# Performance work log

Measured on AMD Instinct MI355X. Metric: run time of the kernel, lower is better.

## Reference

```python
import jax, jax.numpy as jnp
import numpy as np
from jax import lax

B, C, O, K, KS, H, W = 16, 256, 256, 4, 3, 64, 64
PAD = 1
BN_EPS = 1e-3


def setup_inputs() -> dict:
    key = jax.random.key(0)
    k1, k2, k3 = jax.random.split(key, 3)
    x = jax.random.normal(k1, (B, C, H, W), dtype=jnp.float32)
    # nn.Parameter(torch.randn(...)) -> standard normal init
    dyn_kernels = jax.random.normal(k2, (K, O, C, KS, KS), dtype=jnp.float32)
    # attention 1x1 conv (no bias): weight [K, C, 1, 1] -> store as [K, C]
    attn_w = jax.random.normal(k3, (K, C), dtype=jnp.float32) / np.sqrt(C).astype(np.float32)
    gamma = jnp.ones((O,), dtype=jnp.float32)
    beta = jnp.zeros((O,), dtype=jnp.float32)
    return {"x": x, "dyn_kernels": dyn_kernels, "attn_w": attn_w, "gamma": gamma, "beta": beta}


def reference(x, dyn_kernels, attn_w, gamma, beta):
    b, c, h, w = x.shape
    k, o = dyn_kernels.shape[0], dyn_kernels.shape[1]
    # attention: global avg pool -> 1x1 conv (no bias) -> softmax over kernels
    pooled = x.mean(axis=(2, 3))                      # [B, C]
    attn = jax.nn.softmax(pooled @ attn_w.T, axis=1)  # [B, K]
    # run all K kernels as a single conv with K*O output channels
    kern = dyn_kernels.reshape(k * o, c, KS, KS)
    y = lax.conv_general_dilated(
        x, kern, window_strides=(1, 1), padding=((PAD, PAD), (PAD, PAD)),
        dimension_numbers=("NCHW", "OIHW", "NCHW"))   # [B, K*O, H, W]
    y = y.reshape(b, k, o, h, w)
    out = jnp.einsum("bkohw,bk->bohw", y, attn)        # weighted sum over kernels
    # BatchNorm2d (training mode: batch statistics, biased variance)
    mean = out.mean(axis=(0, 2, 3))
    var = out.var(axis=(0, 2, 3))
    inv = gamma * lax.rsqrt(var + BN_EPS)
    out = (out - mean[None, :, None, None]) * inv[None, :, None, None] + beta[None, :, None, None]
    # SiLU
    return out * jax.nn.sigmoid(out)
```

## Files before the change

### kernel.cpp

```cpp
#include <hip/hip_runtime.h>
#include <math.h>


#define B_ 16
#define C_ 256
#define O_ 256
#define HW_ 4096
#define PLANE_F4 1024
#define WPERK 589824
#define XS_PX 40

typedef short bf16x8 __attribute__((ext_vector_type(8)));
typedef float f32x4 __attribute__((ext_vector_type(4)));

__device__ __forceinline__ unsigned short f2bf(float f) {
    unsigned u = __float_as_uint(f);
    u += 0x7FFFu + ((u >> 16) & 1u);
    return (unsigned short)(u >> 16);
}
__device__ __forceinline__ float bf2f(unsigned short h) {
    return __uint_as_float((unsigned)h << 16);
}

__global__ __launch_bounds__(256) void pool_kernel(const float4* __restrict__ x4,
                                                   float* __restrict__ pooled) {
    int bc = blockIdx.x;
    const float4* p = x4 + (size_t)bc * PLANE_F4;
    float s = 0.f;
    for (int i = threadIdx.x; i < PLANE_F4; i += 256) {
        float4 v = p[i];
        s += v.x + v.y + v.z + v.w;
    }
    for (int off = 32; off; off >>= 1) s += __shfl_down(s, off);
    __shared__ float partial[4];
    if ((threadIdx.x & 63) == 0) partial[threadIdx.x >> 6] = s;
    __syncthreads();
    if (threadIdx.x == 0)
        pooled[bc] = (partial[0] + partial[1] + partial[2] + partial[3]) * (1.f / 4096.f);
}

__global__ void attn_kernel(const float* __restrict__ pooled,
                            const float* __restrict__ attn_w,
                            float* __restrict__ attn) {
    int tid = threadIdx.x;
    int b = tid >> 2, k = tid & 3;
    float s = 0.f;
    for (int c = 0; c < C_; ++c) s += pooled[b * C_ + c] * attn_w[k * C_ + c];
    __shared__ float lg[16][4];
    lg[b][k] = s;
    __syncthreads();
    float m = fmaxf(fmaxf(lg[b][0], lg[b][1]), fmaxf(lg[b][2], lg[b][3]));
    float den = expf(lg[b][0] - m) + expf(lg[b][1] - m) +
                expf(lg[b][2] - m) + expf(lg[b][3] - m);
    attn[tid] = expf(s - m) / den;
}

__global__ __launch_bounds__(256) void wtrans_kernel(const float* __restrict__ dyn,
                                                     const float* __restrict__ attn,
                                                     unsigned short* __restrict__ wt_hi,
                                                     unsigned short* __restrict__ wt_lo) {
    int idx = blockIdx.x * 256 + threadIdx.x;
    int b = idx >> 16;
    int o = (idx >> 8) & 255;
    int c = idx & 255;
    float a0 = attn[b * 4 + 0], a1 = attn[b * 4 + 1],
          a2 = attn[b * 4 + 2], a3 = attn[b * 4 + 3];
    const float* p0 = dyn + ((size_t)o * 256 + c) * 9;
    float v[9];
#pragma unroll
    for (int t = 0; t < 9; ++t)
        v[t] = a0 * p0[t] + a1 * p0[WPERK + t] + a2 * p0[2 * WPERK + t] + a3 * p0[3 * WPERK + t];
    size_t obase = ((size_t)(b * 256 + o) * 9) * 256 + c;
#pragma unroll
    for (int t = 0; t < 9; ++t) {
        float f = v[t];
        unsigned short h = f2bf(f);
        unsigned short l = f2bf(f - bf2f(h));
        wt_hi[obase + (size_t)t * 256] = h;
        wt_lo[obase + (size_t)t * 256] = l;
    }
}

__global__ __launch_bounds__(256, 2) void conv_mfma_kernel(const float* __restrict__ x,
        const unsigned short* __restrict__ wt_hi,
        const unsigned short* __restrict__ wt_lo,
        float* __restrict__ out) {
    __shared__ __align__(16) unsigned short xs_hi[4 * 66 * XS_PX];
    __shared__ __align__(16) unsigned short xs_lo[4 * 66 * XS_PX];

    const int h0   = blockIdx.x * 2;
    const int ob   = blockIdx.y * 128;
    const int b    = blockIdx.z;
    const int tid  = threadIdx.x;
    const int lane = tid & 63;
    const int wid  = tid >> 6;
    const int lo16 = lane & 15;
    const int g    = lane >> 4;
    const int wo   = ob + (wid >> 1) * 64;
    const int hr   = h0 + (wid & 1);

    const float* xb = x + (size_t)b * (C_ * HW_);

    f32x4 acc[4][4];
#pragma unroll
    for (int i = 0; i < 4; ++i)
#pragma unroll
        for (int j = 0; j < 4; ++j) acc[i][j] = (f32x4){0.f, 0.f, 0.f, 0.f};

    const unsigned short* wph = wt_hi + ((size_t)(b * 256 + wo + lo16) * 9) * 256 + g * 8;
    const unsigned short* wpl = wt_lo + ((size_t)(b * 256 + wo + lo16) * 9) * 256 + g * 8;
    const unsigned short* xh = xs_hi + ((wid & 1) * 66 + lo16) * XS_PX + g * 8;
    const unsigned short* xl = xs_lo + ((wid & 1) * 66 + lo16) * XS_PX + g * 8;

#pragma unroll 1
    for (int cb = 0; cb < 256; cb += 32) {
        __syncthreads();
        for (int it = tid; it < 4 * 264; it += 256) {
            int cchunk = it / 264;
            int px = it - cchunk * 264;
            int r = px / 66;
            int w = px - r * 66;
            int hh = h0 - 1 + r;
            int ww = w - 1;
            unsigned hi_w[4] = {0u, 0u, 0u, 0u}, lo_w[4] = {0u, 0u, 0u, 0u};
            if ((unsigned)hh < 64u && (unsigned)ww < 64u) {
                const float* xp = xb + (size_t)(cb + cchunk * 8) * HW_ + hh * 64 + ww;
#pragma unroll
                for (int i = 0; i < 8; ++i) {
                    float f = xp[(size_t)i * HW_];
                    unsigned short h = f2bf(f);
                    unsigned short l = f2bf(f - bf2f(h));
                    hi_w[i >> 1] |= (unsigned)h << ((i & 1) * 16);
                    lo_w[i >> 1] |= (unsigned)l << ((i & 1) * 16);
                }
            }
            int off = px * XS_PX + cchunk * 8;
            *(uint4*)&xs_hi[off] = make_uint4(hi_w[0], hi_w[1], hi_w[2], hi_w[3]);
            *(uint4*)&xs_lo[off] = make_uint4(lo_w[0], lo_w[1], lo_w[2], lo_w[3]);
        }
        __syncthreads();

#pragma unroll
        for (int t = 0; t < 9; ++t) {
            const int dh = t / 3, dw = t % 3;
            bf16x8 bh[4], bl[4];
#pragma unroll
            for (int nf = 0; nf < 4; ++nf) {
                const int xoff = (dh * 66 + dw + nf * 16) * XS_PX;
                bh[nf] = *(const bf16x8*)&xh[xoff];
                bl[nf] = *(const bf16x8*)&xl[xoff];
            }
#pragma unroll
            for (int mf = 0; mf < 4; ++mf) {
                const size_t woff = (size_t)(mf * 16 * 9 + t) * 256 + cb;
                bf16x8 ah = *(const bf16x8*)(wph + woff);
                bf16x8 al = *(const bf16x8*)(wpl + woff);
#pragma unroll
                for (int nf = 0; nf < 4; ++nf) {
                    acc[mf][nf] = __builtin_amdgcn_mfma_f32_16x16x32_bf16(ah, bh[nf], acc[mf][nf], 0, 0, 0);
                    acc[mf][nf] = __builtin_amdgcn_mfma_f32_16x16x32_bf16(ah, bl[nf], acc[mf][nf], 0, 0, 0);
                    acc[mf][nf] = __builtin_amdgcn_mfma_f32_16x16x32_bf16(al, bh[nf], acc[mf][nf], 0, 0, 0);
                }
            }
        }
    }

    float* op = out + ((size_t)b * 256 + wo) * HW_ + (size_t)hr * 64;
#pragma unroll
    for (int mf = 0; mf < 4; ++mf)
#pragma unroll
        for (int nf = 0; nf < 4; ++nf) {
            f32x4 a = acc[mf][nf];
#pragma unroll
            for (int r = 0; r < 4; ++r)
                op[(size_t)(mf * 16 + g * 4 + r) * HW_ + nf * 16 + lo16] = a[r];
        }
}

template <bool OTF>
__global__ __launch_bounds__(256, 2) void conv_kernel(const float* __restrict__ x,
                                                      const float* __restrict__ wsrc,
                                                      const float* __restrict__ attn,
                                                      float* __restrict__ out) {
    __shared__ __align__(16) float xs[8][3][72];
    __shared__ __align__(16) float wsh[64 * 100];

    const int h   = blockIdx.x;
    const int ob  = blockIdx.y * 64;
    const int b   = blockIdx.z;
    const int tid = threadIdx.x;
    const int o_idx = tid >> 4;
    const int w0    = (tid & 15) * 4;

    float a0 = 0.f, a1 = 0.f, a2 = 0.f, a3 = 0.f;
    if (OTF) {
        a0 = attn[b * 4 + 0]; a1 = attn[b * 4 + 1];
        a2 = attn[b * 4 + 2]; a3 = attn[b * 4 + 3];
    }
    const float* xb = x + (size_t)b * (C_ * HW_);
    const float* wb = OTF ? (wsrc + (size_t)ob * 2304)
                          : (wsrc + (size_t)b * WPERK + (size_t)ob * 2304);
    float acc[4][4];
#pragma unroll
    for (int i = 0; i < 4; ++i)
#pragma unroll
        for (int j = 0; j < 4; ++j) acc[i][j] = 0.f;

    for (int cb = 0; cb < C_; cb += 8) {
        __syncthreads();
        for (int idx = tid; idx < 8 * 3 * 66; idx += 256) {
            int c = idx / 198, rem = idx - c * 198;
            int r = rem / 66, wi = rem - r * 66;
            int hh = h - 1 + r, ww = wi - 1;
            float v = 0.f;
            if ((unsigned)hh < 64u && (unsigned)ww < 64u)
                v = xb[(size_t)(cb + c) * HW_ + hh * 64 + ww];
            xs[c][r][wi] = v;
        }
        for (int idx = tid; idx < 64 * 72; idx += 256) {
            int o = idx / 72, j = idx - o * 72;
            int c = j / 9, t = j - c * 9;
            size_t gi = (size_t)o * 2304 + (size_t)(cb + c) * 9 + t;
            float v;
            if (OTF)
                v = a0 * wb[gi] + a1 * wb[WPERK + gi] +
                    a2 * wb[2 * WPERK + gi] + a3 * wb[3 * WPERK + gi];
            else
                v = wb[gi];
            wsh[o * 100 + c * 12 + t] = v;
        }
        __syncthreads();
#pragma unroll
        for (int cc = 0; cc < 8; ++cc) {
            float xr[3][6];
#pragma unroll
            for (int r = 0; r < 3; ++r) {
                float4 a = *(const float4*)&xs[cc][r][w0];
                float2 b2 = *(const float2*)&xs[cc][r][w0 + 4];
                xr[r][0] = a.x; xr[r][1] = a.y; xr[r][2] = a.z; xr[r][3] = a.w;
                xr[r][4] = b2.x; xr[r][5] = b2.y;
            }
#pragma unroll
            for (int oo = 0; oo < 4; ++oo) {
                const float* wp = &wsh[(o_idx * 4 + oo) * 100 + cc * 12];
                float4 wA = *(const float4*)wp;
                float4 wB = *(const float4*)(wp + 4);
                float w8 = wp[8];
#pragma unroll
                for (int ww = 0; ww < 4; ++ww) {
                    acc[oo][ww] += wA.x * xr[0][ww]     + wA.y * xr[0][ww + 1] + wA.z * xr[0][ww + 2]
                                 + wA.w * xr[1][ww]     + wB.x * xr[1][ww + 1] + wB.y * xr[1][ww + 2]
                                 + wB.z * xr[2][ww]     + wB.w * xr[2][ww + 1] + w8   * xr[2][ww + 2];
                }
            }
        }
    }
    float* op = out + ((size_t)b * O_ + ob) * HW_ + h * 64;
#pragma unroll
    for (int oo = 0; oo < 4; ++oo) {
        float4 v = make_float4(acc[oo][0], acc[oo][1], acc[oo][2], acc[oo][3]);
        *(float4*)&op[(size_t)(o_idx * 4 + oo) * HW_ + w0] = v;
    }
}

__global__ __launch_bounds__(256) void stats_kernel(const float4* __restrict__ out4,
                                                    const float* __restrict__ gamma,
                                                    float* __restrict__ mean,
                                                    float* __restrict__ inv) {
    int o = blockIdx.x;
    float s = 0.f, s2 = 0.f;
    for (int b = 0; b < B_; ++b) {
        const float4* p = out4 + ((size_t)b * O_ + o) * PLANE_F4;
        for (int i = threadIdx.x; i < PLANE_F4; i += 256) {
            float4 v = p[i];
            s  += v.x + v.y + v.z + v.w;
            s2 += v.x * v.x + v.y * v.y + v.z * v.z + v.w * v.w;
        }
    }
    for (int off = 32; off; off >>= 1) {
        s  += __shfl_down(s, off);
        s2 += __shfl_down(s2, off);
    }
    __shared__ float ps[4], ps2[4];
    int w = threadIdx.x >> 6;
    if ((threadIdx.x & 63) == 0) { ps[w] = s; ps2[w] = s2; }
    __syncthreads();
    if (threadIdx.x == 0) {
        float S = ps[0] + ps[1] + ps[2] + ps[3];
        float S2 = ps2[0] + ps2[1] + ps2[2] + ps2[3];
        float m = S * (1.f / 65536.f);
        float var = S2 * (1.f / 65536.f) - m * m;
        mean[o] = m;
        inv[o] = gamma[o] * rsqrtf(var + 1e-3f);
    }
}

__global__ __launch_bounds__(256) void bn_silu_kernel(float4* __restrict__ out4,
                                                      const float* __restrict__ mean,
                                                      const float* __restrict__ inv,
                                                      const float* __restrict__ beta) {
    const int total = B_ * O_ * PLANE_F4;
    for (int i = blockIdx.x * 256 + threadIdx.x; i < total; i += gridDim.x * 256) {
        int plane = i >> 10;
        int o = plane & 255;
        float m = mean[o], iv = inv[o], bt = beta[o];
        float4 v = out4[i];
        float u;
        u = (v.x - m) * iv + bt; v.x = u / (1.f + expf(-u));
        u = (v.y - m) * iv + bt; v.y = u / (1.f + expf(-u));
        u = (v.z - m) * iv + bt; v.z = u / (1.f + expf(-u));
        u = (v.w - m) * iv + bt; v.w = u / (1.f + expf(-u));
        out4[i] = v;
    }
}

extern "C" void kernel_launch(void* const* d_in, const int* in_sizes, int n_in,
                              void* d_out, int out_size, void* d_ws, size_t ws_size,
                              hipStream_t stream) {
    const float* x      = (const float*)d_in[0];
    const float* dyn    = (const float*)d_in[1];
    const float* attn_w = (const float*)d_in[2];
    const float* gamma  = (const float*)d_in[3];
    const float* beta   = (const float*)d_in[4];
    float* out = (float*)d_out;
    float* ws  = (float*)d_ws;

    float* pooled = ws;
    float* attn   = ws + 4096;
    float* mean   = ws + 4160;
    float* inv    = ws + 4416;
    unsigned short* wt_hi = (unsigned short*)(ws + 4672);
    unsigned short* wt_lo = wt_hi + 9437184;

    const size_t needed = (size_t)4672 * 4 + 2ull * 9437184ull * 2ull;
    const bool mfma_path = ws_size >= needed;

    pool_kernel<<<4096, 256, 0, stream>>>((const float4*)x, pooled);
    attn_kernel<<<1, 64, 0, stream>>>(pooled, attn_w, attn);
    if (mfma_path) {
        wtrans_kernel<<<4096, 256, 0, stream>>>(dyn, attn, wt_hi, wt_lo);
        conv_mfma_kernel<<<dim3(32, 2, 16), 256, 0, stream>>>(x, wt_hi, wt_lo, out);
    } else {
        conv_kernel<true><<<dim3(64, 4, 16), 256, 0, stream>>>(x, dyn, attn, out);
    }
    stats_kernel<<<256, 256, 0, stream>>>((const float4*)out, gamma, mean, inv);
    bn_silu_kernel<<<4096, 256, 0, stream>>>((float4*)out, mean, inv, beta);
}
```

Baseline: 518.7 us.

## Switch conv to 32x32 MFMA, register-prefetch input staging, swizzle grid, split BN stats

The conv kernel now uses 32x32x16 bf16 MFMAs with 2x2 accumulator tiles instead of 16x16x32, which cuts LDS fragment reads per MFMA. Input staging is simplified so each thread loads one pixel column for 32 channels into registers one chunk ahead and stores it after a barrier, overlapping global loads with MFMA compute. The grid becomes 1D with a swizzle so that blocks scheduled together spread across batches and row tiles. BN statistics are split into a 4096-block per-plane reduction plus a tiny finalize kernel to raise parallelism, with the partial sums reusing the weight scratch buffer after the conv finishes. The register prefetch raises register pressure, which may hurt occupancy.

```diff
diff --git a/kernel.cpp b/kernel.cpp
--- a/kernel.cpp
+++ b/kernel.cpp
@@ -11,7 +11,7 @@
 #define XS_PX 40
 
 typedef short bf16x8 __attribute__((ext_vector_type(8)));
-typedef float f32x4 __attribute__((ext_vector_type(4)));
+typedef float f32x16 __attribute__((ext_vector_type(16)));
 
 __device__ __forceinline__ unsigned short f2bf(float f) {
     unsigned u = __float_as_uint(f);
@@ -88,145 +88,198 @@
     __shared__ __align__(16) unsigned short xs_hi[4 * 66 * XS_PX];
     __shared__ __align__(16) unsigned short xs_lo[4 * 66 * XS_PX];
 
-    const int h0   = blockIdx.x * 2;
-    const int ob   = blockIdx.y * 128;
-    const int b    = blockIdx.z;
+    const int bid = blockIdx.x;
+    const int swz = (bid & 7) * 128 + (bid >> 3);
+    const int b  = swz >> 6;
+    const int ob = (swz >> 5) & 1;
+    const int hp = swz & 31;
+    const int h0 = hp * 2;
+
     const int tid  = threadIdx.x;
     const int lane = tid & 63;
     const int wid  = tid >> 6;
-    const int lo16 = lane & 15;
-    const int g    = lane >> 4;
-    const int wo   = ob + (wid >> 1) * 64;
-    const int hr   = h0 + (wid & 1);
-
-    const float* xb = x + (size_t)b * (C_ * HW_);
-
-    f32x4 acc[4][4];
-#pragma unroll
-    for (int i = 0; i < 4; ++i)
-#pragma unroll
-        for (int j = 0; j < 4; ++j) acc[i][j] = (f32x4){0.f, 0.f, 0.f, 0.f};
-
-    const unsigned short* wph = wt_hi + ((size_t)(b * 256 + wo + lo16) * 9) * 256 + g * 8;
-    const unsigned short* wpl = wt_lo + ((size_t)(b * 256 + wo + lo16) * 9) * 256 + g * 8;
-    const unsigned short* xh = xs_hi + ((wid & 1) * 66 + lo16) * XS_PX + g * 8;
-    const unsigned short* xl = xs_lo + ((wid & 1) * 66 + lo16) * XS_PX + g * 8;
-
+    const int l31  = lane & 31;
+    const int g2   = lane >> 5;
+    const int wo   = ob * 128 + (wid >> 1) * 64;
+    const int wrow = wid & 1;
+    const int hr   = h0 + wrow;
+
+    const int sr = wid;
+    const int sw = lane;
+    const int hh = h0 - 1 + sr;
+    const bool hvalid = (unsigned)hh < 64u;
+    const float* xsrc = x + (size_t)b * (C_ * HW_) + (size_t)(hvalid ? hh : 0) * 64 + sw;
+    unsigned short* sh_hi = &xs_hi[(sr * 66 + sw + 1) * XS_PX];
+    unsigned short* sh_lo = &xs_lo[(sr * 66 + sw + 1) * XS_PX];
+
+    if (tid < 8) {
+        int r = tid >> 1;
+        int slot = r * 66 + ((tid & 1) ? 65 : 0);
+        uint4 z = make_uint4(0u, 0u, 0u, 0u);
+#pragma unroll
+        for (int u = 0; u < 4; ++u) {
+            *(uint4*)&xs_hi[slot * XS_PX + u * 8] = z;
+            *(uint4*)&xs_lo[slot * XS_PX + u * 8] = z;
+        }
+    }
+
+    f32x16 acc[2][2];
+#pragma unroll
+    for (int i = 0; i < 2; ++i)
+#pragma unroll
+        for (int j = 0; j < 2; ++j) acc[i][j] = (f32x16)(0.f);
+
+    const unsigned short* wbh = wt_hi + ((size_t)(b * 256 + wo + l31) * 9) * 256 + g2 * 8;
+    const unsigned short* wbl = wt_lo + ((size_t)(b * 256 + wo + l31) * 9) * 256 + g2 * 8;
+    const unsigned short* xph = xs_hi + (wrow * 66 + l31) * XS_PX + g2 * 8;
+    const unsigned short* xpl = xs_lo + (wrow * 66 + l31) * XS_PX + g2 * 8;
+
+#define LOADX(buf, cb) do {                                              \
+        const float* _p = xsrc + (size_t)(cb) * HW_;                     \
+        if (hvalid) {                                                    \
+            _Pragma("unroll")                                            \
+            for (int _c = 0; _c < 32; ++_c) buf[_c] = _p[(size_t)_c * HW_]; \
+        } else {                                                         \
+            _Pragma("unroll")                                            \
+            for (int _c = 0; _c < 32; ++_c) buf[_c] = 0.f;               \
+        }                                                                \
+    } while (0)
+
+#define STOREX(buf) do {                                                 \
+        unsigned _hw[16], _lw[16];                                       \
+        _Pragma("unroll")                                                \
+        for (int _c = 0; _c < 16; ++_c) {                                \
+            unsigned short h0_ = f2bf(buf[2 * _c]);                      \
+            unsigned short l0_ = f2bf(buf[2 * _c] - bf2f(h0_));          \
+            unsigned short h1_ = f2bf(buf[2 * _c + 1]);                  \
+            unsigned short l1_ = f2bf(buf[2 * _c + 1] - bf2f(h1_));      \
+            _hw[_c] = (unsigned)h0_ | ((unsigned)h1_ << 16);             \
+            _lw[_c] = (unsigned)l0_ | ((unsigned)l1_ << 16);             \
+        }                                                                \
+        _Pragma("unroll")                                                \
+        for (int _u = 0; _u < 4; ++_u) {                                 \
+            *(uint4*)&sh_hi[_u * 8] = make_uint4(_hw[4*_u], _hw[4*_u+1], _hw[4*_u+2], _hw[4*_u+3]); \
+            *(uint4*)&sh_lo[_u * 8] = make_uint4(_lw[4*_u], _lw[4*_u+1], _lw[4*_u+2], _lw[4*_u+3]); \
+        }                                                                \
+    } while (0)
+
+#define MFMA_CHUNK(cb) do {                                              \
+        _Pragma("unroll")                                                \
+        for (int t = 0; t < 9; ++t) {                                    \
+            const int dh = t / 3, dw = t % 3;                            \
+            bf16x8 bh_[2][2], bl_[2][2];                                 \
+            _Pragma("unroll")                                            \
+            for (int ks = 0; ks < 2; ++ks)                               \
+                _Pragma("unroll")                                        \
+                for (int nf = 0; nf < 2; ++nf) {                         \
+                    const int xoff = (dh * 66 + dw + nf * 32) * XS_PX + ks * 16; \
+                    bh_[ks][nf] = *(const bf16x8*)&xph[xoff];            \
+                    bl_[ks][nf] = *(const bf16x8*)&xpl[xoff];            \
+                }                                                        \
+            bf16x8 ah_[2][2], al_[2][2];                                 \
+            _Pragma("unroll")                                            \
+            for (int mf = 0; mf < 2; ++mf)                               \
+                _Pragma("unroll")                                        \
+                for (int ks = 0; ks < 2; ++ks) {                         \
+                    const size_t woff = (size_t)mf * 73728 + (size_t)t * 256 + ks * 16 + (cb); \
+                    ah_[mf][ks] = *(const bf16x8*)(wbh + woff);          \
+                    al_[mf][ks] = *(const bf16x8*)(wbl + woff);          \
+                }                                                        \
+            _Pragma("unroll")                                            \
+            for (int mf = 0; mf < 2; ++mf)                               \
+                _Pragma("unroll")                                        \
+                for (int ks = 0; ks < 2; ++ks)                           \
+                    _Pragma("unroll")                                    \
+                    for (int nf = 0; nf < 2; ++nf)                       \
+                        acc[mf][nf] = __builtin_amdgcn_mfma_f32_32x32x16_bf16(ah_[mf][ks], bh_[ks][nf], acc[mf][nf], 0, 0, 0); \
+            _Pragma("unroll")                                            \
+            for (int mf = 0; mf < 2; ++mf)                               \
+                _Pragma("unroll")                                        \
+                for (int ks = 0; ks < 2; ++ks)                           \
+                    _Pragma("unroll")                                    \
+                    for (int nf = 0; nf < 2; ++nf)                       \
+                        acc[mf][nf] = __builtin_amdgcn_mfma_f32_32x32x16_bf16(ah_[mf][ks], bl_[ks][nf], acc[mf][nf], 0, 0, 0); \
+            _Pragma("unroll")                                            \
+            for (int mf = 0; mf < 2; ++mf)                               \
+                _Pragma("unroll")                                        \
+                for (int ks = 0; ks < 2; ++ks)                           \
+                    _Pragma("unroll")                                    \
+                    for (int nf = 0; nf < 2; ++nf)                       \
+                        acc[mf][nf] = __builtin_amdgcn_mfma_f32_32x32x16_bf16(al_[mf][ks], bh_[ks][nf], acc[mf][nf], 0, 0, 0); \
+        }                                                                \
+    } while (0)
+
+    float xa[32], xb2[32];
+    LOADX(xa, 0);
 #pragma unroll 1
-    for (int cb = 0; cb < 256; cb += 32) {
-        __syncthreads();
-        for (int it = tid; it < 4 * 264; it += 256) {
-            int cchunk = it / 264;
-            int px = it - cchunk * 264;
-            int r = px / 66;
-            int w = px - r * 66;
-            int hh = h0 - 1 + r;
-            int ww = w - 1;
-            unsigned hi_w[4] = {0u, 0u, 0u, 0u}, lo_w[4] = {0u, 0u, 0u, 0u};
-            if ((unsigned)hh < 64u && (unsigned)ww < 64u) {
-                const float* xp = xb + (size_t)(cb + cchunk * 8) * HW_ + hh * 64 + ww;
-#pragma unroll
-                for (int i = 0; i < 8; ++i) {
-                    float f = xp[(size_t)i * HW_];
-                    unsigned short h = f2bf(f);
-                    unsigned short l = f2bf(f - bf2f(h));
-                    hi_w[i >> 1] |= (unsigned)h << ((i & 1) * 16);
-                    lo_w[i >> 1] |= (unsigned)l << ((i & 1) * 16);
-                }
-            }
-            int off = px * XS_PX + cchunk * 8;
-            *(uint4*)&xs_hi[off] = make_uint4(hi_w[0], hi_w[1], hi_w[2], hi_w[3]);
-            *(uint4*)&xs_lo[off] = make_uint4(lo_w[0], lo_w[1], lo_w[2], lo_w[3]);
-        }
-        __syncthreads();
-
-#pragma unroll
-        for (int t = 0; t < 9; ++t) {
-            const int dh = t / 3, dw = t % 3;
-            bf16x8 bh[4], bl[4];
-#pragma unroll
-            for (int nf = 0; nf < 4; ++nf) {
-                const int xoff = (dh * 66 + dw + nf * 16) * XS_PX;
-                bh[nf] = *(const bf16x8*)&xh[xoff];
-                bl[nf] = *(const bf16x8*)&xl[xoff];
-            }
-#pragma unroll
-            for (int mf = 0; mf < 4; ++mf) {
-                const size_t woff = (size_t)(mf * 16 * 9 + t) * 256 + cb;
-                bf16x8 ah = *(const bf16x8*)(wph + woff);
-                bf16x8 al = *(const bf16x8*)(wpl + woff);
-#pragma unroll
-                for (int nf = 0; nf < 4; ++nf) {
-                    acc[mf][nf] = __builtin_amdgcn_mfma_f32_16x16x32_bf16(ah, bh[nf], acc[mf][nf], 0, 0, 0);
-                    acc[mf][nf] = __builtin_amdgcn_mfma_f32_16x16x32_bf16(ah, bl[nf], acc[mf][nf], 0, 0, 0);
-                    acc[mf][nf] = __builtin_amdgcn_mfma_f32_16x16x32_bf16(al, bh[nf], acc[mf][nf], 0, 0, 0);
-                }
+    for (int cc = 0; cc < 256; cc += 64) {
+        __syncthreads();
+        STOREX(xa);
+        __syncthreads();
+        LOADX(xb2, cc + 32);
+        MFMA_CHUNK(cc);
+        __syncthreads();
+        STOREX(xb2);
+        __syncthreads();
+        if (cc + 64 < 256) LOADX(xa, cc + 64);
+        MFMA_CHUNK(cc + 32);
+    }
+
+    float* op = out + ((size_t)b * 256 + wo) * HW_ + (size_t)hr * 64;
+#pragma unroll
+    for (int mf = 0; mf < 2; ++mf)
+#pragma unroll
+        for (int nf = 0; nf < 2; ++nf) {
+            f32x16 a = acc[mf][nf];
+#pragma unroll
+            for (int r = 0; r < 16; ++r) {
+                int row = (r & 3) + 8 * (r >> 2) + 4 * g2;
+                op[(size_t)(mf * 32 + row) * HW_ + nf * 32 + l31] = a[r];
             }
         }
-    }
-
-    float* op = out + ((size_t)b * 256 + wo) * HW_ + (size_t)hr * 64;
-#pragma unroll
-    for (int mf = 0; mf < 4; ++mf)
-#pragma unroll
-        for (int nf = 0; nf < 4; ++nf) {
-            f32x4 a = acc[mf][nf];
-#pragma unroll
-            for (int r = 0; r < 4; ++r)
-                op[(size_t)(mf * 16 + g * 4 + r) * HW_ + nf * 16 + lo16] = a[r];
-        }
-}
-
-template <bool OTF>
-__global__ __launch_bounds__(256, 2) void conv_kernel(const float* __restrict__ x,
-                                                      const float* __restrict__ wsrc,
-                                                      const float* __restrict__ attn,
-                                                      float* __restrict__ out) {
+#undef LOADX
+#undef STOREX
+#undef MFMA_CHUNK
+}
+
+__global__ __launch_bounds__(256, 2) void conv_otf_kernel(const float* __restrict__ x,
+                                                          const float* __restrict__ wsrc,
+                                                          const float* __restrict__ attn,
+                                                          float* __restrict__ out) {
     __shared__ __align__(16) float xs[8][3][72];
     __shared__ __align__(16) float wsh[64 * 100];
-
     const int h   = blockIdx.x;
     const int ob  = blockIdx.y * 64;
     const int b   = blockIdx.z;
     const int tid = threadIdx.x;
     const int o_idx = tid >> 4;
     const int w0    = (tid & 15) * 4;
-
-    float a0 = 0.f, a1 = 0.f, a2 = 0.f, a3 = 0.f;
-    if (OTF) {
-        a0 = attn[b * 4 + 0]; a1 = attn[b * 4 + 1];
-        a2 = attn[b * 4 + 2]; a3 = attn[b * 4 + 3];
-    }
+    float a0 = attn[b * 4 + 0], a1 = attn[b * 4 + 1],
+          a2 = attn[b * 4 + 2], a3 = attn[b * 4 + 3];
     const float* xb = x + (size_t)b * (C_ * HW_);
-    const float* wb = OTF ? (wsrc + (size_t)ob * 2304)
-                          : (wsrc + (size_t)b * WPERK + (size_t)ob * 2304);
+    const float* wb = wsrc + (size_t)ob * 2304;
     float acc[4][4];
 #pragma unroll
     for (int i = 0; i < 4; ++i)
 #pragma unroll
         for (int j = 0; j < 4; ++j) acc[i][j] = 0.f;
-
     for (int cb = 0; cb < C_; cb += 8) {
         __syncthreads();
         for (int idx = tid; idx < 8 * 3 * 66; idx += 256) {
             int c = idx / 198, rem = idx - c * 198;
             int r = rem / 66, wi = rem - r * 66;
-            int hh = h - 1 + r, ww = wi - 1;
+            int hhh = h - 1 + r, ww = wi - 1;
             float v = 0.f;
-            if ((unsigned)hh < 64u && (unsigned)ww < 64u)
-                v = xb[(size_t)(cb + c) * HW_ + hh * 64 + ww];
+            if ((unsigned)hhh < 64u && (unsigned)ww < 64u)
+                v = xb[(size_t)(cb + c) * HW_ + hhh * 64 + ww];
             xs[c][r][wi] = v;
         }
         for (int idx = tid; idx < 64 * 72; idx += 256) {
             int o = idx / 72, j = idx - o * 72;
             int c = j / 9, t = j - c * 9;
             size_t gi = (size_t)o * 2304 + (size_t)(cb + c) * 9 + t;
-            float v;
-            if (OTF)
-                v = a0 * wb[gi] + a1 * wb[WPERK + gi] +
-                    a2 * wb[2 * WPERK + gi] + a3 * wb[3 * WPERK + gi];
-            else
-                v = wb[gi];
+            float v = a0 * wb[gi] + a1 * wb[WPERK + gi] +
+                      a2 * wb[2 * WPERK + gi] + a3 * wb[3 * WPERK + gi];
             wsh[o * 100 + c * 12 + t] = v;
         }
         __syncthreads();
@@ -263,19 +316,16 @@
     }
 }
 
-__global__ __launch_bounds__(256) void stats_kernel(const float4* __restrict__ out4,
-                                                    const float* __restrict__ gamma,
-                                                    float* __restrict__ mean,
-                                                    float* __restrict__ inv) {
-    int o = blockIdx.x;
+__global__ __launch_bounds__(256) void stats1_kernel(const float4* __restrict__ out4,
+                                                     float* __restrict__ psum,
+                                                     float* __restrict__ psumsq) {
+    int bo = blockIdx.x;
+    const float4* p = out4 + (size_t)bo * PLANE_F4;
     float s = 0.f, s2 = 0.f;
-    for (int b = 0; b < B_; ++b) {
-        const float4* p = out4 + ((size_t)b * O_ + o) * PLANE_F4;
-        for (int i = threadIdx.x; i < PLANE_F4; i += 256) {
-            float4 v = p[i];
-            s  += v.x + v.y + v.z + v.w;
-            s2 += v.x * v.x + v.y * v.y + v.z * v.z + v.w * v.w;
-        }
+    for (int i = threadIdx.x; i < PLANE_F4; i += 256) {
+        float4 v = p[i];
+        s  += v.x + v.y + v.z + v.w;
+        s2 += v.x * v.x + v.y * v.y + v.z * v.z + v.w * v.w;
     }
     for (int off = 32; off; off >>= 1) {
         s  += __shfl_down(s, off);
@@ -286,13 +336,27 @@
     if ((threadIdx.x & 63) == 0) { ps[w] = s; ps2[w] = s2; }
     __syncthreads();
     if (threadIdx.x == 0) {
-        float S = ps[0] + ps[1] + ps[2] + ps[3];
-        float S2 = ps2[0] + ps2[1] + ps2[2] + ps2[3];
-        float m = S * (1.f / 65536.f);
-        float var = S2 * (1.f / 65536.f) - m * m;
-        mean[o] = m;
-        inv[o] = gamma[o] * rsqrtf(var + 1e-3f);
-    }
+        psum[bo]   = ps[0] + ps[1] + ps[2] + ps[3];
+        psumsq[bo] = ps2[0] + ps2[1] + ps2[2] + ps2[3];
+    }
+}
+
+__global__ __launch_bounds__(256) void stats2_kernel(const float* __restrict__ psum,
+                                                     const float* __restrict__ psumsq,
+                                                     const float* __restrict__ gamma,
+                                                     float* __restrict__ mean,
+                                                     float* __restrict__ inv) {
+    int o = threadIdx.x;
+    float S = 0.f, S2 = 0.f;
+#pragma unroll
+    for (int b = 0; b < B_; ++b) {
+        S  += psum[b * 256 + o];
+        S2 += psumsq[b * 256 + o];
+    }
+    float m = S * (1.f / 65536.f);
+    float var = S2 * (1.f / 65536.f) - m * m;
+    mean[o] = m;
+    inv[o] = gamma[o] * rsqrtf(var + 1e-3f);
 }
 
 __global__ __launch_bounds__(256) void bn_silu_kernel(float4* __restrict__ out4,
@@ -331,6 +395,8 @@
     float* inv    = ws + 4416;
     unsigned short* wt_hi = (unsigned short*)(ws + 4672);
     unsigned short* wt_lo = wt_hi + 9437184;
+    float* psum   = (float*)wt_hi;
+    float* psumsq = psum + 4096;
 
     const size_t needed = (size_t)4672 * 4 + 2ull * 9437184ull * 2ull;
     const bool mfma_path = ws_size >= needed;
@@ -339,10 +405,11 @@
     attn_kernel<<<1, 64, 0, stream>>>(pooled, attn_w, attn);
     if (mfma_path) {
         wtrans_kernel<<<4096, 256, 0, stream>>>(dyn, attn, wt_hi, wt_lo);
-        conv_mfma_kernel<<<dim3(32, 2, 16), 256, 0, stream>>>(x, wt_hi, wt_lo, out);
+        conv_mfma_kernel<<<1024, 256, 0, stream>>>(x, wt_hi, wt_lo, out);
     } else {
-        conv_kernel<true><<<dim3(64, 4, 16), 256, 0, stream>>>(x, dyn, attn, out);
-    }
-    stats_kernel<<<256, 256, 0, stream>>>((const float4*)out, gamma, mean, inv);
+        conv_otf_kernel<<<dim3(64, 4, 16), 256, 0, stream>>>(x, dyn, attn, out);
+    }
+    stats1_kernel<<<4096, 256, 0, stream>>>((const float4*)out, psum, psumsq);
+    stats2_kernel<<<1, 256, 0, stream>>>(psum, psumsq, gamma, mean, inv);
     bn_silu_kernel<<<4096, 256, 0, stream>>>((float4*)out, mean, inv, beta);
 }
```

Result: faster. 450.0 us (-13.2%).
